# Performance work log

Hardware: AMD Instinct MI355X
Metric: run time of the kernel (lower is better)

## Reference

```python
import jax, jax.numpy as jnp
import numpy as np

B, S, H, D = 8, 1024, 16, 64
EMBED_DIM = H * D  # 1024
NEG_INF = -1e30


def setup_inputs() -> dict:
    key = jax.random.key(0)
    kq, kk, kv, kl = jax.random.split(key, 4)
    q = jax.random.normal(kq, (B, S, H, D), dtype=jnp.float32)
    k = jax.random.normal(kk, (B, S, H, D), dtype=jnp.float32)
    v = jax.random.normal(kv, (B, S, H, D), dtype=jnp.float32)
    # ragged lengths in [S//4, S]; prefix-style key_padding_mask (True = valid)
    lengths = jax.random.randint(kl, (B,), S // 4, S + 1)
    key_padding_mask = jnp.arange(S)[None, :] < lengths[:, None]
    return {"q": q, "k": k, "v": v, "key_padding_mask": key_padding_mask}


def reference(q, k, v, key_padding_mask):
    # Equivalent math of flash_attn_unpadded_qkvpacked_func on unpadded tokens
    # followed by pad_input (zeros at padded query rows), dropout=0 (eval).
    # NOTE: module uses softmax_scale = embed_dim ** -0.5 (not head_dim).
    scale = EMBED_DIM ** (-0.5)
    scores = jnp.einsum("bqhd,bkhd->bhqk", q, k) * scale  # [B,H,S,S]
    scores = jnp.where(key_padding_mask[:, None, None, :], scores, NEG_INF)
    attn = jax.nn.softmax(scores, axis=-1)
    out = jnp.einsum("bhqk,bkhd->bqhd", attn, v)  # [B,S,H,D]
    # pad_input re-inserts zeros at padded query positions
    out = out * key_padding_mask[:, :, None, None].astype(out.dtype)
    return out.reshape(B, S, H * D)
```

## Files before the change

kernel.cpp:

```cpp
#include <hip/hip_runtime.h>


#define SS 1024
#define NH 16
#define DD 64
#define ROWSTRIDE (NH * DD)
#define SCALE 0.03125f
#define LOG2E 1.4426950408889634f
#define PC1 (SCALE * LOG2E)
#define PC2 (-12.0f * LOG2E)
#define KSTR 72
#define VSTR 72

typedef short bf16x8 __attribute__((ext_vector_type(8)));
typedef unsigned short u16;
typedef unsigned short u16x8 __attribute__((ext_vector_type(8)));
typedef unsigned short u16x4 __attribute__((ext_vector_type(4)));
typedef float f32x4 __attribute__((ext_vector_type(4)));
typedef unsigned u32x4 __attribute__((ext_vector_type(4)));

__device__ __forceinline__ u16 f2bf(float x) {
  unsigned u = __builtin_bit_cast(unsigned, x);
  return (u16)((u + 0x7FFFu + ((u >> 16) & 1u)) >> 16);
}
__device__ __forceinline__ float bf2f(u16 s) {
  unsigned u = ((unsigned)s) << 16;
  return __builtin_bit_cast(float, u);
}
__device__ __forceinline__ unsigned pkbf(float a, float b) {
#if __has_builtin(__builtin_amdgcn_cvt_pk_bf16_f32)
  auto r = __builtin_amdgcn_cvt_pk_bf16_f32(a, b);
  return __builtin_bit_cast(unsigned, r);
#else
  return (unsigned)f2bf(a) | ((unsigned)f2bf(b) << 16);
#endif
}

__global__ __launch_bounds__(256, 4) void fa_main(const void* qv, const void* kv,
                                                  const void* vv, const void* maskv,
                                                  float* out) {
  __shared__ __attribute__((aligned(16))) u16 Kt[64 * KSTR];
  __shared__ __attribute__((aligned(16))) u16 Vt[64 * VSTR + 64];

  int tid = threadIdx.x;
  int lane = tid & 63;
  int w = tid >> 6;
  int t = lane & 15;
  int quad = lane >> 4;

  int bid = blockIdx.x;
  int x = bid & 7;
  int j = bid >> 3;
  int g = j >> 4;
  int r = j & 15;
  int qt = (r + g) & 15;
  int bh = (g << 3) + x;
  int h = bh & (NH - 1);
  int b = bh >> 4;
  int q0 = qt * 64;

  const u16* qs16 = (const u16*)qv;
  float dv = bf2f(qs16[2 * lane]);
  unsigned long long bal = __ballot(!(fabsf(dv) < 100.0f));
  int isf32 = (__popcll(bal) >= 16) ? 1 : 0;

  const unsigned char* m8 = (const unsigned char*)maskv;
  const int* m32 = (const int*)maskv;
  bool isu8 = (m8[1] != 0);
  int lo = 0, hi = SS;
  while (lo < hi) {
    int mid = (lo + hi) >> 1;
    int vbit = isu8 ? (m8[b * SS + mid] != 0) : (m32[b * SS + mid] != 0);
    if (vbit) lo = mid + 1; else hi = mid;
  }
  int len = lo;

  size_t base = (size_t)b * SS * ROWSTRIDE + h * DD;

  if (q0 >= len) {
    f32x4 z4 = {0.f, 0.f, 0.f, 0.f};
    for (int i = tid; i < 64 * 16; i += 256) {
      int r2 = i >> 4, dseg = (i & 15) << 2;
      *(f32x4*)&out[base + (size_t)(q0 + r2) * ROWSTRIDE + dseg] = z4;
    }
    return;
  }

  int qrow = q0 + w * 16 + t;
  bf16x8 qf[2];
  if (isf32) {
    const float* qp = (const float*)qv + base + (size_t)qrow * ROWSTRIDE + quad * 8;
#pragma unroll
    for (int kk = 0; kk < 2; kk++) {
      union { bf16x8 v; unsigned d[4]; } u;
#pragma unroll
      for (int jj = 0; jj < 4; jj++)
        u.d[jj] = pkbf(qp[kk * 32 + 2 * jj], qp[kk * 32 + 2 * jj + 1]);
      qf[kk] = u.v;
    }
  } else {
    const u16* qp = (const u16*)qv + base + (size_t)qrow * ROWSTRIDE + quad * 8;
#pragma unroll
    for (int kk = 0; kk < 2; kk++) qf[kk] = *(const bf16x8*)(qp + kk * 32);
  }

  f32x4 zero4 = {0.f, 0.f, 0.f, 0.f};
  f32x4 oacc[4];
#pragma unroll
  for (int c = 0; c < 4; c++) oacc[c] = zero4;
  float lsum = 0.f;

  int key = tid >> 2, seg = tid & 3;
  int kp = tid >> 3, ds = tid & 7;
  int nkt = (len + 63) >> 6;

  f32x4 kA[4], vA[4];
  u16x8 kB[2], vB[2];

  auto issue_loads = [&](int kt) {
    int krow = kt * 64 + key;
    if (krow > SS - 1) krow = SS - 1;
    int vrow = kt * 64 + 2 * kp;
    if (vrow > SS - 2) vrow = SS - 2;
    size_t ksrc = base + (size_t)krow * ROWSTRIDE + seg * 16;
    size_t vsrc = base + (size_t)vrow * ROWSTRIDE + ds * 8;
    if (isf32) {
      const f32x4* kpp = (const f32x4*)((const float*)kv + ksrc);
#pragma unroll
      for (int i = 0; i < 4; i++) kA[i] = kpp[i];
      const float* vp = (const float*)vv + vsrc;
      vA[0] = *(const f32x4*)vp;
      vA[1] = *(const f32x4*)(vp + 4);
      vA[2] = *(const f32x4*)(vp + ROWSTRIDE);
      vA[3] = *(const f32x4*)(vp + ROWSTRIDE + 4);
    } else {
      const u16x8* kpp = (const u16x8*)((const u16*)kv + ksrc);
      kB[0] = kpp[0]; kB[1] = kpp[1];
      const u16* vp = (const u16*)vv + vsrc;
      vB[0] = *(const u16x8*)vp;
      vB[1] = *(const u16x8*)(vp + ROWSTRIDE);
    }
  };

  auto stage_to_lds = [&]() {
    if (isf32) {
      unsigned kd[8];
#pragma unroll
      for (int i = 0; i < 8; i++)
        kd[i] = pkbf(kA[i >> 1][2 * (i & 1)], kA[i >> 1][2 * (i & 1) + 1]);
      *(u32x4*)&Kt[key * KSTR + seg * 16] = u32x4{kd[0], kd[1], kd[2], kd[3]};
      *(u32x4*)&Kt[key * KSTR + seg * 16 + 8] = u32x4{kd[4], kd[5], kd[6], kd[7]};
#pragma unroll
      for (int jj = 0; jj < 8; jj++) {
        int d = ds * 8 + jj;
        *(unsigned*)&Vt[d * VSTR + (d >> 4) * 16 + 2 * kp] =
            pkbf(vA[jj >> 2][jj & 3], vA[2 + (jj >> 2)][jj & 3]);
      }
    } else {
      *(u16x8*)&Kt[key * KSTR + seg * 16] = kB[0];
      *(u16x8*)&Kt[key * KSTR + seg * 16 + 8] = kB[1];
#pragma unroll
      for (int jj = 0; jj < 8; jj++) {
        int d = ds * 8 + jj;
        *(unsigned*)&Vt[d * VSTR + (d >> 4) * 16 + 2 * kp] =
            (unsigned)(u16)vB[0][jj] | ((unsigned)(u16)vB[1][jj] << 16);
      }
    }
  };

  issue_loads(0);

  for (int kt = 0; kt < nkt; ++kt) {
    __syncthreads();
    stage_to_lds();
    if (kt + 1 < nkt) issue_loads(kt + 1);
    __syncthreads();

    f32x4 sacc[4];
#pragma unroll
    for (int c = 0; c < 4; c++) sacc[c] = zero4;
#pragma unroll
    for (int kk = 0; kk < 2; kk++) {
#pragma unroll
      for (int c = 0; c < 4; c++) {
        bf16x8 ka = *(const bf16x8*)&Kt[(c * 16 + t) * KSTR + kk * 32 + quad * 8];
        sacc[c] = __builtin_amdgcn_mfma_f32_16x16x32_bf16(ka, qf[kk], sacc[c], 0, 0, 0);
      }
    }

    float p[4][4];
    if (kt == nkt - 1) {
      int krem = len - kt * 64;
#pragma unroll
      for (int c = 0; c < 4; c++) {
        int kbase = c * 16 + quad * 4;
#pragma unroll
        for (int rr = 0; rr < 4; rr++)
          p[c][rr] = (kbase + rr < krem)
                         ? __builtin_amdgcn_exp2f(fmaf(sacc[c][rr], PC1, PC2))
                         : 0.0f;
      }
    } else {
#pragma unroll
      for (int c = 0; c < 4; c++)
#pragma unroll
        for (int rr = 0; rr < 4; rr++)
          p[c][rr] = __builtin_amdgcn_exp2f(fmaf(sacc[c][rr], PC1, PC2));
    }
#pragma unroll
    for (int c = 0; c < 4; c++)
      lsum += (p[c][0] + p[c][1]) + (p[c][2] + p[c][3]);

    unsigned pd[4][2];
#pragma unroll
    for (int c = 0; c < 4; c++) {
      pd[c][0] = pkbf(p[c][0], p[c][1]);
      pd[c][1] = pkbf(p[c][2], p[c][3]);
    }

#pragma unroll
    for (int kc = 0; kc < 2; kc++) {
      union { bf16x8 v; unsigned d[4]; } pa;
      pa.d[0] = pd[2 * kc][0];
      pa.d[1] = pd[2 * kc][1];
      pa.d[2] = pd[2 * kc + 1][0];
      pa.d[3] = pd[2 * kc + 1][1];
#pragma unroll
      for (int c = 0; c < 4; c++) {
        const u16* vr = &Vt[(c * 16 + t) * VSTR + c * 16 + kc * 32 + quad * 4];
        union { bf16x8 v; u16x4 h[2]; } vb;
        vb.h[0] = *(const u16x4*)vr;
        vb.h[1] = *(const u16x4*)(vr + 16);
        oacc[c] = __builtin_amdgcn_mfma_f32_16x16x32_bf16(pa.v, vb.v, oacc[c], 0, 0, 0);
      }
    }
  }

  lsum += __shfl_xor(lsum, 16);
  lsum += __shfl_xor(lsum, 32);
  float inv[4];
#pragma unroll
  for (int rr = 0; rr < 4; rr++)
    inv[rr] = 1.0f / __shfl(lsum, quad * 4 + rr);
#pragma unroll
  for (int c = 0; c < 4; c++)
#pragma unroll
    for (int rr = 0; rr < 4; rr++) {
      int qr = q0 + w * 16 + quad * 4 + rr;
      float o = oacc[c][rr] * inv[rr];
      out[base + (size_t)qr * ROWSTRIDE + c * 16 + t] = (qr < len) ? o : 0.0f;
    }
}

extern "C" void kernel_launch(void* const* d_in, const int* in_sizes, int n_in,
                              void* d_out, int out_size, void* d_ws, size_t ws_size,
                              hipStream_t stream) {
  fa_main<<<2048, 256, 0, stream>>>(d_in[0], d_in[1], d_in[2], d_in[3], (float*)d_out);
}
```

Baseline: 170.5 us.

## Double-buffer K/V shared tiles and raise wave priority around MFMA blocks

Splits the K and V LDS tiles into two buffers. The next tile is staged into the idle buffer while the current one feeds the MFMAs, which cuts the loop from two barriers per iteration to one. Global loads are now issued two tiles ahead. The MFMA sections are also wrapped in s_setprio to favour matrix work. LDS use doubles to about 37 KB per block, which may lower occupancy, and the extra prefetch depth raises register pressure.

```diff
diff --git a/kernel.cpp b/kernel.cpp
--- a/kernel.cpp
+++ b/kernel.cpp
@@ -39,8 +39,8 @@
 __global__ __launch_bounds__(256, 4) void fa_main(const void* qv, const void* kv,
                                                   const void* vv, const void* maskv,
                                                   float* out) {
-  __shared__ __attribute__((aligned(16))) u16 Kt[64 * KSTR];
-  __shared__ __attribute__((aligned(16))) u16 Vt[64 * VSTR + 64];
+  __shared__ __attribute__((aligned(16))) u16 Kt[2][64 * KSTR];
+  __shared__ __attribute__((aligned(16))) u16 Vt[2][64 * VSTR + 64];
 
   int tid = threadIdx.x;
   int lane = tid & 63;
@@ -142,51 +142,60 @@
     }
   };
 
-  auto stage_to_lds = [&]() {
+  auto stage_to_lds = [&](int bsel) {
+    u16* KtB = &Kt[bsel][0];
+    u16* VtB = &Vt[bsel][0];
     if (isf32) {
       unsigned kd[8];
 #pragma unroll
       for (int i = 0; i < 8; i++)
         kd[i] = pkbf(kA[i >> 1][2 * (i & 1)], kA[i >> 1][2 * (i & 1) + 1]);
-      *(u32x4*)&Kt[key * KSTR + seg * 16] = u32x4{kd[0], kd[1], kd[2], kd[3]};
-      *(u32x4*)&Kt[key * KSTR + seg * 16 + 8] = u32x4{kd[4], kd[5], kd[6], kd[7]};
+      *(u32x4*)&KtB[key * KSTR + seg * 16] = u32x4{kd[0], kd[1], kd[2], kd[3]};
+      *(u32x4*)&KtB[key * KSTR + seg * 16 + 8] = u32x4{kd[4], kd[5], kd[6], kd[7]};
 #pragma unroll
       for (int jj = 0; jj < 8; jj++) {
         int d = ds * 8 + jj;
-        *(unsigned*)&Vt[d * VSTR + (d >> 4) * 16 + 2 * kp] =
+        *(unsigned*)&VtB[d * VSTR + (d >> 4) * 16 + 2 * kp] =
             pkbf(vA[jj >> 2][jj & 3], vA[2 + (jj >> 2)][jj & 3]);
       }
     } else {
-      *(u16x8*)&Kt[key * KSTR + seg * 16] = kB[0];
-      *(u16x8*)&Kt[key * KSTR + seg * 16 + 8] = kB[1];
+      *(u16x8*)&KtB[key * KSTR + seg * 16] = kB[0];
+      *(u16x8*)&KtB[key * KSTR + seg * 16 + 8] = kB[1];
 #pragma unroll
       for (int jj = 0; jj < 8; jj++) {
         int d = ds * 8 + jj;
-        *(unsigned*)&Vt[d * VSTR + (d >> 4) * 16 + 2 * kp] =
+        *(unsigned*)&VtB[d * VSTR + (d >> 4) * 16 + 2 * kp] =
             (unsigned)(u16)vB[0][jj] | ((unsigned)(u16)vB[1][jj] << 16);
       }
     }
   };
 
   issue_loads(0);
+  stage_to_lds(0);
+  if (nkt > 1) issue_loads(1);
+  __syncthreads();
 
   for (int kt = 0; kt < nkt; ++kt) {
-    __syncthreads();
-    stage_to_lds();
-    if (kt + 1 < nkt) issue_loads(kt + 1);
-    __syncthreads();
+    int cur = kt & 1, nxt = cur ^ 1;
+    if (kt + 1 < nkt) stage_to_lds(nxt);
+    if (kt + 2 < nkt) issue_loads(kt + 2);
+
+    const u16* KtC = &Kt[cur][0];
+    const u16* VtC = &Vt[cur][0];
 
     f32x4 sacc[4];
 #pragma unroll
     for (int c = 0; c < 4; c++) sacc[c] = zero4;
+    __builtin_amdgcn_s_setprio(1);
 #pragma unroll
     for (int kk = 0; kk < 2; kk++) {
 #pragma unroll
       for (int c = 0; c < 4; c++) {
-        bf16x8 ka = *(const bf16x8*)&Kt[(c * 16 + t) * KSTR + kk * 32 + quad * 8];
+        bf16x8 ka = *(const bf16x8*)&KtC[(c * 16 + t) * KSTR + kk * 32 + quad * 8];
         sacc[c] = __builtin_amdgcn_mfma_f32_16x16x32_bf16(ka, qf[kk], sacc[c], 0, 0, 0);
       }
     }
+    __builtin_amdgcn_s_setprio(0);
 
     float p[4][4];
     if (kt == nkt - 1) {
@@ -218,6 +227,7 @@
       pd[c][1] = pkbf(p[c][2], p[c][3]);
     }
 
+    __builtin_amdgcn_s_setprio(1);
 #pragma unroll
     for (int kc = 0; kc < 2; kc++) {
       union { bf16x8 v; unsigned d[4]; } pa;
@@ -227,13 +237,16 @@
       pa.d[3] = pd[2 * kc + 1][1];
 #pragma unroll
       for (int c = 0; c < 4; c++) {
-        const u16* vr = &Vt[(c * 16 + t) * VSTR + c * 16 + kc * 32 + quad * 4];
+        const u16* vr = &VtC[(c * 16 + t) * VSTR + c * 16 + kc * 32 + quad * 4];
         union { bf16x8 v; u16x4 h[2]; } vb;
         vb.h[0] = *(const u16x4*)vr;
         vb.h[1] = *(const u16x4*)(vr + 16);
         oacc[c] = __builtin_amdgcn_mfma_f32_16x16x32_bf16(pa.v, vb.v, oacc[c], 0, 0, 0);
       }
     }
+    __builtin_amdgcn_s_setprio(0);
+
+    __syncthreads();
   }
 
   lsum += __shfl_xor(lsum, 16);
```

Result: no change. 170.1 us (-0.2%).

## Process two query tiles per block to reuse each staged K/V tile

Applied to the files above, without the earlier changes.

Each block now handles two 64-row query tiles (p and p+8) against the same staged K/V tiles in LDS, which halves the global K/V loads and conversions per query tile. The grid is halved to 1024 blocks, and a compile-time template flag picks a single-tile path when the second tile is fully padded. It also raises wave priority with s_setprio around the MFMA sections. The cost is more registers per thread, which may lower occupancy, and fewer blocks to balance the ragged lengths across CUs.

```diff
diff --git a/kernel.cpp b/kernel.cpp
--- a/kernel.cpp
+++ b/kernel.cpp
@@ -19,6 +19,9 @@
 typedef float f32x4 __attribute__((ext_vector_type(4)));
 typedef unsigned u32x4 __attribute__((ext_vector_type(4)));
 
+struct TrueT { static constexpr bool value = true; };
+struct FalseT { static constexpr bool value = false; };
+
 __device__ __forceinline__ u16 f2bf(float x) {
   unsigned u = __builtin_bit_cast(unsigned, x);
   return (u16)((u + 0x7FFFu + ((u >> 16) & 1u)) >> 16);
@@ -51,13 +54,14 @@
   int bid = blockIdx.x;
   int x = bid & 7;
   int j = bid >> 3;
-  int g = j >> 4;
-  int r = j & 15;
-  int qt = (r + g) & 15;
+  int rslot = j & 7;
+  int g = j >> 3;
+  int p = (rslot + g) & 7;
   int bh = (g << 3) + x;
   int h = bh & (NH - 1);
   int b = bh >> 4;
-  int q0 = qt * 64;
+  int q0A = p * 64;
+  int q0B = (p + 8) * 64;
 
   const u16* qs16 = (const u16*)qv;
   float dv = bf2f(qs16[2 * lane]);
@@ -77,38 +81,46 @@
 
   size_t base = (size_t)b * SS * ROWSTRIDE + h * DD;
 
-  if (q0 >= len) {
+  auto zslab = [&](int q0) {
     f32x4 z4 = {0.f, 0.f, 0.f, 0.f};
     for (int i = tid; i < 64 * 16; i += 256) {
       int r2 = i >> 4, dseg = (i & 15) << 2;
       *(f32x4*)&out[base + (size_t)(q0 + r2) * ROWSTRIDE + dseg] = z4;
     }
-    return;
-  }
-
-  int qrow = q0 + w * 16 + t;
-  bf16x8 qf[2];
-  if (isf32) {
-    const float* qp = (const float*)qv + base + (size_t)qrow * ROWSTRIDE + quad * 8;
-#pragma unroll
-    for (int kk = 0; kk < 2; kk++) {
-      union { bf16x8 v; unsigned d[4]; } u;
-#pragma unroll
-      for (int jj = 0; jj < 4; jj++)
-        u.d[jj] = pkbf(qp[kk * 32 + 2 * jj], qp[kk * 32 + 2 * jj + 1]);
-      qf[kk] = u.v;
-    }
-  } else {
-    const u16* qp = (const u16*)qv + base + (size_t)qrow * ROWSTRIDE + quad * 8;
-#pragma unroll
-    for (int kk = 0; kk < 2; kk++) qf[kk] = *(const bf16x8*)(qp + kk * 32);
-  }
+  };
+
+  bool liveA = q0A < len;
+  bool liveB = q0B < len;
+  if (!liveA) { zslab(q0A); zslab(q0B); return; }
+  if (!liveB) zslab(q0B);
+
+  auto load_q = [&](int q0, bf16x8 qf[2]) {
+    int qrow = q0 + w * 16 + t;
+    if (isf32) {
+      const float* qp = (const float*)qv + base + (size_t)qrow * ROWSTRIDE + quad * 8;
+#pragma unroll
+      for (int kk = 0; kk < 2; kk++) {
+        union { bf16x8 v; unsigned d[4]; } u;
+#pragma unroll
+        for (int jj = 0; jj < 4; jj++)
+          u.d[jj] = pkbf(qp[kk * 32 + 2 * jj], qp[kk * 32 + 2 * jj + 1]);
+        qf[kk] = u.v;
+      }
+    } else {
+      const u16* qp = (const u16*)qv + base + (size_t)qrow * ROWSTRIDE + quad * 8;
+#pragma unroll
+      for (int kk = 0; kk < 2; kk++) qf[kk] = *(const bf16x8*)(qp + kk * 32);
+    }
+  };
+  bf16x8 qfA[2], qfB[2];
+  load_q(q0A, qfA);
+  if (liveB) load_q(q0B, qfB);
 
   f32x4 zero4 = {0.f, 0.f, 0.f, 0.f};
-  f32x4 oacc[4];
-#pragma unroll
-  for (int c = 0; c < 4; c++) oacc[c] = zero4;
-  float lsum = 0.f;
+  f32x4 oaccA[4], oaccB[4];
+#pragma unroll
+  for (int c = 0; c < 4; c++) { oaccA[c] = zero4; oaccB[c] = zero4; }
+  float lsumA = 0.f, lsumB = 0.f;
 
   int key = tid >> 2, seg = tid & 3;
   int kp = tid >> 3, ds = tid & 7;
@@ -168,92 +180,112 @@
     }
   };
 
-  issue_loads(0);
-
-  for (int kt = 0; kt < nkt; ++kt) {
-    __syncthreads();
-    stage_to_lds();
-    if (kt + 1 < nkt) issue_loads(kt + 1);
-    __syncthreads();
-
-    f32x4 sacc[4];
-#pragma unroll
-    for (int c = 0; c < 4; c++) sacc[c] = zero4;
-#pragma unroll
-    for (int kk = 0; kk < 2; kk++) {
-#pragma unroll
-      for (int c = 0; c < 4; c++) {
-        bf16x8 ka = *(const bf16x8*)&Kt[(c * 16 + t) * KSTR + kk * 32 + quad * 8];
-        sacc[c] = __builtin_amdgcn_mfma_f32_16x16x32_bf16(ka, qf[kk], sacc[c], 0, 0, 0);
-      }
-    }
-
-    float p[4][4];
-    if (kt == nkt - 1) {
+  auto kloop = [&](auto DOBT) {
+    constexpr bool DOB = decltype(DOBT)::value;
+    issue_loads(0);
+    for (int kt = 0; kt < nkt; ++kt) {
+      __syncthreads();
+      stage_to_lds();
+      if (kt + 1 < nkt) issue_loads(kt + 1);
+      __syncthreads();
+
+      f32x4 saccA[4], saccB[4];
+#pragma unroll
+      for (int c = 0; c < 4; c++) { saccA[c] = zero4; if constexpr (DOB) saccB[c] = zero4; }
+      __builtin_amdgcn_s_setprio(1);
+#pragma unroll
+      for (int kk = 0; kk < 2; kk++) {
+#pragma unroll
+        for (int c = 0; c < 4; c++) {
+          bf16x8 ka = *(const bf16x8*)&Kt[(c * 16 + t) * KSTR + kk * 32 + quad * 8];
+          saccA[c] = __builtin_amdgcn_mfma_f32_16x16x32_bf16(ka, qfA[kk], saccA[c], 0, 0, 0);
+          if constexpr (DOB)
+            saccB[c] = __builtin_amdgcn_mfma_f32_16x16x32_bf16(ka, qfB[kk], saccB[c], 0, 0, 0);
+        }
+      }
+      __builtin_amdgcn_s_setprio(0);
+
+      unsigned pdA[4][2], pdB[4][2];
+      bool lastt = (kt == nkt - 1);
       int krem = len - kt * 64;
 #pragma unroll
       for (int c = 0; c < 4; c++) {
         int kbase = c * 16 + quad * 4;
-#pragma unroll
-        for (int rr = 0; rr < 4; rr++)
-          p[c][rr] = (kbase + rr < krem)
-                         ? __builtin_amdgcn_exp2f(fmaf(sacc[c][rr], PC1, PC2))
-                         : 0.0f;
-      }
-    } else {
-#pragma unroll
-      for (int c = 0; c < 4; c++)
-#pragma unroll
-        for (int rr = 0; rr < 4; rr++)
-          p[c][rr] = __builtin_amdgcn_exp2f(fmaf(sacc[c][rr], PC1, PC2));
-    }
+        float pa[4], pb[4];
+        if (lastt) {
+#pragma unroll
+          for (int rr = 0; rr < 4; rr++) {
+            bool in = (kbase + rr < krem);
+            pa[rr] = in ? __builtin_amdgcn_exp2f(fmaf(saccA[c][rr], PC1, PC2)) : 0.0f;
+            if constexpr (DOB)
+              pb[rr] = in ? __builtin_amdgcn_exp2f(fmaf(saccB[c][rr], PC1, PC2)) : 0.0f;
+          }
+        } else {
+#pragma unroll
+          for (int rr = 0; rr < 4; rr++) {
+            pa[rr] = __builtin_amdgcn_exp2f(fmaf(saccA[c][rr], PC1, PC2));
+            if constexpr (DOB)
+              pb[rr] = __builtin_amdgcn_exp2f(fmaf(saccB[c][rr], PC1, PC2));
+          }
+        }
+        lsumA += (pa[0] + pa[1]) + (pa[2] + pa[3]);
+        pdA[c][0] = pkbf(pa[0], pa[1]);
+        pdA[c][1] = pkbf(pa[2], pa[3]);
+        if constexpr (DOB) {
+          lsumB += (pb[0] + pb[1]) + (pb[2] + pb[3]);
+          pdB[c][0] = pkbf(pb[0], pb[1]);
+          pdB[c][1] = pkbf(pb[2], pb[3]);
+        }
+      }
+
+      __builtin_amdgcn_s_setprio(1);
+#pragma unroll
+      for (int kc = 0; kc < 2; kc++) {
+        union { bf16x8 v; unsigned d[4]; } paA, paB;
+        paA.d[0] = pdA[2 * kc][0]; paA.d[1] = pdA[2 * kc][1];
+        paA.d[2] = pdA[2 * kc + 1][0]; paA.d[3] = pdA[2 * kc + 1][1];
+        if constexpr (DOB) {
+          paB.d[0] = pdB[2 * kc][0]; paB.d[1] = pdB[2 * kc][1];
+          paB.d[2] = pdB[2 * kc + 1][0]; paB.d[3] = pdB[2 * kc + 1][1];
+        }
+#pragma unroll
+        for (int c = 0; c < 4; c++) {
+          const u16* vr = &Vt[(c * 16 + t) * VSTR + c * 16 + kc * 32 + quad * 4];
+          union { bf16x8 v; u16x4 h[2]; } vb;
+          vb.h[0] = *(const u16x4*)vr;
+          vb.h[1] = *(const u16x4*)(vr + 16);
+          oaccA[c] = __builtin_amdgcn_mfma_f32_16x16x32_bf16(paA.v, vb.v, oaccA[c], 0, 0, 0);
+          if constexpr (DOB)
+            oaccB[c] = __builtin_amdgcn_mfma_f32_16x16x32_bf16(paB.v, vb.v, oaccB[c], 0, 0, 0);
+        }
+      }
+      __builtin_amdgcn_s_setprio(0);
+    }
+  };
+  if (liveB) kloop(TrueT{}); else kloop(FalseT{});
+
+  auto write_tile = [&](float lsum, f32x4 oacc[4], int q0) {
+    lsum += __shfl_xor(lsum, 16);
+    lsum += __shfl_xor(lsum, 32);
+    float inv[4];
+#pragma unroll
+    for (int rr = 0; rr < 4; rr++)
+      inv[rr] = 1.0f / __shfl(lsum, quad * 4 + rr);
 #pragma unroll
     for (int c = 0; c < 4; c++)
-      lsum += (p[c][0] + p[c][1]) + (p[c][2] + p[c][3]);
-
-    unsigned pd[4][2];
-#pragma unroll
-    for (int c = 0; c < 4; c++) {
-      pd[c][0] = pkbf(p[c][0], p[c][1]);
-      pd[c][1] = pkbf(p[c][2], p[c][3]);
-    }
-
-#pragma unroll
-    for (int kc = 0; kc < 2; kc++) {
-      union { bf16x8 v; unsigned d[4]; } pa;
-      pa.d[0] = pd[2 * kc][0];
-      pa.d[1] = pd[2 * kc][1];
-      pa.d[2] = pd[2 * kc + 1][0];
-      pa.d[3] = pd[2 * kc + 1][1];
-#pragma unroll
-      for (int c = 0; c < 4; c++) {
-        const u16* vr = &Vt[(c * 16 + t) * VSTR + c * 16 + kc * 32 + quad * 4];
-        union { bf16x8 v; u16x4 h[2]; } vb;
-        vb.h[0] = *(const u16x4*)vr;
-        vb.h[1] = *(const u16x4*)(vr + 16);
-        oacc[c] = __builtin_amdgcn_mfma_f32_16x16x32_bf16(pa.v, vb.v, oacc[c], 0, 0, 0);
-      }
-    }
-  }
-
-  lsum += __shfl_xor(lsum, 16);
-  lsum += __shfl_xor(lsum, 32);
-  float inv[4];
-#pragma unroll
-  for (int rr = 0; rr < 4; rr++)
-    inv[rr] = 1.0f / __shfl(lsum, quad * 4 + rr);
-#pragma unroll
-  for (int c = 0; c < 4; c++)
-#pragma unroll
-    for (int rr = 0; rr < 4; rr++) {
-      int qr = q0 + w * 16 + quad * 4 + rr;
-      float o = oacc[c][rr] * inv[rr];
-      out[base + (size_t)qr * ROWSTRIDE + c * 16 + t] = (qr < len) ? o : 0.0f;
-    }
+#pragma unroll
+      for (int rr = 0; rr < 4; rr++) {
+        int qr = q0 + w * 16 + quad * 4 + rr;
+        float o = oacc[c][rr] * inv[rr];
+        out[base + (size_t)qr * ROWSTRIDE + c * 16 + t] = (qr < len) ? o : 0.0f;
+      }
+  };
+  write_tile(lsumA, oaccA, q0A);
+  if (liveB) write_tile(lsumB, oaccB, q0B);
 }
 
 extern "C" void kernel_launch(void* const* d_in, const int* in_sizes, int n_in,
                               void* d_out, int out_size, void* d_ws, size_t ws_size,
                               hipStream_t stream) {
-  fa_main<<<2048, 256, 0, stream>>>(d_in[0], d_in[1], d_in[2], d_in[3], (float*)d_out);
-}
+  fa_main<<<1024, 256, 0, stream>>>(d_in[0], d_in[1], d_in[2], d_in[3], (float*)d_out);
+}
```

Measured after the change: 199.7 us. 17.1% more time.

## Halve query tile to 32 rows per block with 128-thread blocks

Applied to the files above, without the earlier changes.

Each block now handles 32 query rows with 2 waves instead of 64 rows with 4 waves, and the grid doubles to 4096 blocks. The K/V staging loop has each thread load two slots so a 64-key tile is still filled. The goal is finer work granularity, which evens out the ragged-length imbalance and skips fully padded query tiles at a finer grain. The cost is that every K/V tile is loaded and converted twice as often overall, doubling global traffic and staging work per query row. The softmax exponent loop is also fused per column chunk.

```diff
diff --git a/kernel.cpp b/kernel.cpp
--- a/kernel.cpp
+++ b/kernel.cpp
@@ -36,7 +36,7 @@
 #endif
 }
 
-__global__ __launch_bounds__(256, 4) void fa_main(const void* qv, const void* kv,
+__global__ __launch_bounds__(128, 4) void fa_main(const void* qv, const void* kv,
                                                   const void* vv, const void* maskv,
                                                   float* out) {
   __shared__ __attribute__((aligned(16))) u16 Kt[64 * KSTR];
@@ -51,13 +51,13 @@
   int bid = blockIdx.x;
   int x = bid & 7;
   int j = bid >> 3;
-  int g = j >> 4;
-  int r = j & 15;
-  int qt = (r + g) & 15;
+  int g = j >> 5;
+  int rslot = j & 31;
+  int slot = (rslot + g) & 31;
   int bh = (g << 3) + x;
   int h = bh & (NH - 1);
   int b = bh >> 4;
-  int q0 = qt * 64;
+  int q0 = slot * 32;
 
   const u16* qs16 = (const u16*)qv;
   float dv = bf2f(qs16[2 * lane]);
@@ -79,7 +79,7 @@
 
   if (q0 >= len) {
     f32x4 z4 = {0.f, 0.f, 0.f, 0.f};
-    for (int i = tid; i < 64 * 16; i += 256) {
+    for (int i = tid; i < 32 * 16; i += 128) {
       int r2 = i >> 4, dseg = (i & 15) << 2;
       *(f32x4*)&out[base + (size_t)(q0 + r2) * ROWSTRIDE + dseg] = z4;
     }
@@ -110,60 +110,70 @@
   for (int c = 0; c < 4; c++) oacc[c] = zero4;
   float lsum = 0.f;
 
-  int key = tid >> 2, seg = tid & 3;
-  int kp = tid >> 3, ds = tid & 7;
   int nkt = (len + 63) >> 6;
 
-  f32x4 kA[4], vA[4];
-  u16x8 kB[2], vB[2];
+  f32x4 kA2[2][4], vA2[2][4];
+  u16x8 kB2[2][2], vB2[2][2];
 
   auto issue_loads = [&](int kt) {
-    int krow = kt * 64 + key;
-    if (krow > SS - 1) krow = SS - 1;
-    int vrow = kt * 64 + 2 * kp;
-    if (vrow > SS - 2) vrow = SS - 2;
-    size_t ksrc = base + (size_t)krow * ROWSTRIDE + seg * 16;
-    size_t vsrc = base + (size_t)vrow * ROWSTRIDE + ds * 8;
-    if (isf32) {
-      const f32x4* kpp = (const f32x4*)((const float*)kv + ksrc);
-#pragma unroll
-      for (int i = 0; i < 4; i++) kA[i] = kpp[i];
-      const float* vp = (const float*)vv + vsrc;
-      vA[0] = *(const f32x4*)vp;
-      vA[1] = *(const f32x4*)(vp + 4);
-      vA[2] = *(const f32x4*)(vp + ROWSTRIDE);
-      vA[3] = *(const f32x4*)(vp + ROWSTRIDE + 4);
-    } else {
-      const u16x8* kpp = (const u16x8*)((const u16*)kv + ksrc);
-      kB[0] = kpp[0]; kB[1] = kpp[1];
-      const u16* vp = (const u16*)vv + vsrc;
-      vB[0] = *(const u16x8*)vp;
-      vB[1] = *(const u16x8*)(vp + ROWSTRIDE);
+#pragma unroll
+    for (int hf = 0; hf < 2; hf++) {
+      int vt = tid + (hf << 7);
+      int key = vt >> 2, seg = vt & 3;
+      int kp = vt >> 3, ds = vt & 7;
+      int krow = kt * 64 + key;
+      if (krow > SS - 1) krow = SS - 1;
+      int vrow = kt * 64 + 2 * kp;
+      if (vrow > SS - 2) vrow = SS - 2;
+      size_t ksrc = base + (size_t)krow * ROWSTRIDE + seg * 16;
+      size_t vsrc = base + (size_t)vrow * ROWSTRIDE + ds * 8;
+      if (isf32) {
+        const f32x4* kpp = (const f32x4*)((const float*)kv + ksrc);
+#pragma unroll
+        for (int i = 0; i < 4; i++) kA2[hf][i] = kpp[i];
+        const float* vp = (const float*)vv + vsrc;
+        vA2[hf][0] = *(const f32x4*)vp;
+        vA2[hf][1] = *(const f32x4*)(vp + 4);
+        vA2[hf][2] = *(const f32x4*)(vp + ROWSTRIDE);
+        vA2[hf][3] = *(const f32x4*)(vp + ROWSTRIDE + 4);
+      } else {
+        const u16x8* kpp = (const u16x8*)((const u16*)kv + ksrc);
+        kB2[hf][0] = kpp[0]; kB2[hf][1] = kpp[1];
+        const u16* vp = (const u16*)vv + vsrc;
+        vB2[hf][0] = *(const u16x8*)vp;
+        vB2[hf][1] = *(const u16x8*)(vp + ROWSTRIDE);
+      }
     }
   };
 
   auto stage_to_lds = [&]() {
-    if (isf32) {
-      unsigned kd[8];
-#pragma unroll
-      for (int i = 0; i < 8; i++)
-        kd[i] = pkbf(kA[i >> 1][2 * (i & 1)], kA[i >> 1][2 * (i & 1) + 1]);
-      *(u32x4*)&Kt[key * KSTR + seg * 16] = u32x4{kd[0], kd[1], kd[2], kd[3]};
-      *(u32x4*)&Kt[key * KSTR + seg * 16 + 8] = u32x4{kd[4], kd[5], kd[6], kd[7]};
-#pragma unroll
-      for (int jj = 0; jj < 8; jj++) {
-        int d = ds * 8 + jj;
-        *(unsigned*)&Vt[d * VSTR + (d >> 4) * 16 + 2 * kp] =
-            pkbf(vA[jj >> 2][jj & 3], vA[2 + (jj >> 2)][jj & 3]);
-      }
-    } else {
-      *(u16x8*)&Kt[key * KSTR + seg * 16] = kB[0];
-      *(u16x8*)&Kt[key * KSTR + seg * 16 + 8] = kB[1];
-#pragma unroll
-      for (int jj = 0; jj < 8; jj++) {
-        int d = ds * 8 + jj;
-        *(unsigned*)&Vt[d * VSTR + (d >> 4) * 16 + 2 * kp] =
-            (unsigned)(u16)vB[0][jj] | ((unsigned)(u16)vB[1][jj] << 16);
+#pragma unroll
+    for (int hf = 0; hf < 2; hf++) {
+      int vt = tid + (hf << 7);
+      int key = vt >> 2, seg = vt & 3;
+      int kp = vt >> 3, ds = vt & 7;
+      if (isf32) {
+        unsigned kd[8];
+#pragma unroll
+        for (int i = 0; i < 8; i++)
+          kd[i] = pkbf(kA2[hf][i >> 1][2 * (i & 1)], kA2[hf][i >> 1][2 * (i & 1) + 1]);
+        *(u32x4*)&Kt[key * KSTR + seg * 16] = u32x4{kd[0], kd[1], kd[2], kd[3]};
+        *(u32x4*)&Kt[key * KSTR + seg * 16 + 8] = u32x4{kd[4], kd[5], kd[6], kd[7]};
+#pragma unroll
+        for (int jj = 0; jj < 8; jj++) {
+          int d = ds * 8 + jj;
+          *(unsigned*)&Vt[d * VSTR + (d >> 4) * 16 + 2 * kp] =
+              pkbf(vA2[hf][jj >> 2][jj & 3], vA2[hf][2 + (jj >> 2)][jj & 3]);
+        }
+      } else {
+        *(u16x8*)&Kt[key * KSTR + seg * 16] = kB2[hf][0];
+        *(u16x8*)&Kt[key * KSTR + seg * 16 + 8] = kB2[hf][1];
+#pragma unroll
+        for (int jj = 0; jj < 8; jj++) {
+          int d = ds * 8 + jj;
+          *(unsigned*)&Vt[d * VSTR + (d >> 4) * 16 + 2 * kp] =
+              (unsigned)(u16)vB2[hf][0][jj] | ((unsigned)(u16)vB2[hf][1][jj] << 16);
+        }
       }
     }
   };
@@ -188,34 +198,27 @@
       }
     }
 
-    float p[4][4];
-    if (kt == nkt - 1) {
-      int krem = len - kt * 64;
-#pragma unroll
-      for (int c = 0; c < 4; c++) {
-        int kbase = c * 16 + quad * 4;
+    unsigned pd[4][2];
+    bool lastt = (kt == nkt - 1);
+    int krem = len - kt * 64;
+#pragma unroll
+    for (int c = 0; c < 4; c++) {
+      int kbase = c * 16 + quad * 4;
+      float p[4];
+      if (lastt) {
 #pragma unroll
         for (int rr = 0; rr < 4; rr++)
-          p[c][rr] = (kbase + rr < krem)
-                         ? __builtin_amdgcn_exp2f(fmaf(sacc[c][rr], PC1, PC2))
-                         : 0.0f;
-      }
-    } else {
-#pragma unroll
-      for (int c = 0; c < 4; c++)
+          p[rr] = (kbase + rr < krem)
+                      ? __builtin_amdgcn_exp2f(fmaf(sacc[c][rr], PC1, PC2))
+                      : 0.0f;
+      } else {
 #pragma unroll
         for (int rr = 0; rr < 4; rr++)
-          p[c][rr] = __builtin_amdgcn_exp2f(fmaf(sacc[c][rr], PC1, PC2));
-    }
-#pragma unroll
-    for (int c = 0; c < 4; c++)
-      lsum += (p[c][0] + p[c][1]) + (p[c][2] + p[c][3]);
-
-    unsigned pd[4][2];
-#pragma unroll
-    for (int c = 0; c < 4; c++) {
-      pd[c][0] = pkbf(p[c][0], p[c][1]);
-      pd[c][1] = pkbf(p[c][2], p[c][3]);
+          p[rr] = __builtin_amdgcn_exp2f(fmaf(sacc[c][rr], PC1, PC2));
+      }
+      lsum += (p[0] + p[1]) + (p[2] + p[3]);
+      pd[c][0] = pkbf(p[0], p[1]);
+      pd[c][1] = pkbf(p[2], p[3]);
     }
 
 #pragma unroll
@@ -255,5 +258,5 @@
 extern "C" void kernel_launch(void* const* d_in, const int* in_sizes, int n_in,
                               void* d_out, int out_size, void* d_ws, size_t ws_size,
                               hipStream_t stream) {
-  fa_main<<<2048, 256, 0, stream>>>(d_in[0], d_in[1], d_in[2], d_in[3], (float*)d_out);
-}
+  fa_main<<<4096, 128, 0, stream>>>(d_in[0], d_in[1], d_in[2], d_in[3], (float*)d_out);
+}
```

New measurement: 318.2 us. 1.87x slower.
